# Performance work log

Measured on AMD Instinct MI355X. Metric: run time of the kernel, lower is better.

## Reference

```python
import jax, jax.numpy as jnp
import numpy as np

N_NODES = 100_000
N_EDGES = 1_600_000
F_IN = 64
H = 200
N_GRAPHS = 512
BN_EPS = 1e-5


def setup_inputs() -> dict:
    key = jax.random.key(0)
    ks = jax.random.split(key, 16)

    def w(k, shape):
        fan_in = shape[0]
        return jax.random.normal(k, shape, jnp.float32) / np.sqrt(fan_in)

    return {
        "x": jax.random.normal(ks[0], (N_NODES, F_IN), jnp.float32),
        "edge_index": jax.random.randint(ks[1], (2, N_EDGES), 0, N_NODES),
        "batch": jnp.sort(jax.random.randint(ks[2], (N_NODES,), 0, N_GRAPHS)),
        "eps1": jnp.zeros((), jnp.float32),
        "W1a": w(ks[3], (F_IN, H)), "b1a": jnp.zeros((H,), jnp.float32),
        "W1b": w(ks[4], (H, H)),    "b1b": jnp.zeros((H,), jnp.float32),
        "bn1_gamma": jnp.ones((H,), jnp.float32), "bn1_beta": jnp.zeros((H,), jnp.float32),
        "bn1_mean": 0.1 * jax.random.normal(ks[5], (H,), jnp.float32),
        "bn1_var": jax.random.uniform(ks[6], (H,), jnp.float32, 0.5, 1.5),
        "eps2": jnp.zeros((), jnp.float32),
        "W2a": w(ks[7], (H, H)), "b2a": jnp.zeros((H,), jnp.float32),
        "W2b": w(ks[8], (H, H)), "b2b": jnp.zeros((H,), jnp.float32),
        "bn2_gamma": jnp.ones((H,), jnp.float32), "bn2_beta": jnp.zeros((H,), jnp.float32),
        "bn2_mean": 0.1 * jax.random.normal(ks[9], (H,), jnp.float32),
        "bn2_var": jax.random.uniform(ks[10], (H,), jnp.float32, 0.5, 1.5),
        "Wfc": w(ks[11], (2 * H, 2)), "bfc": jnp.zeros((2,), jnp.float32),
    }


def _gin_conv(x, edge_index, eps, Wa, ba, Wb, bb):
    # GINConv: MLP((1+eps)*x + sum_{j in N(i)} x_j); messages flow src->dst
    src, dst = edge_index[0], edge_index[1]
    agg = jax.ops.segment_sum(x[src], dst, num_segments=x.shape[0])  # [N, d]
    h = (1.0 + eps) * x + agg
    return jax.nn.relu(h @ Wa + ba) @ Wb + bb


def _bn_eval(h, gamma, beta, mean, var):
    return (h - mean) * jax.lax.rsqrt(var + BN_EPS) * gamma + beta


def reference(x, edge_index, batch, eps1, W1a, b1a, W1b, b1b,
              bn1_gamma, bn1_beta, bn1_mean, bn1_var,
              eps2, W2a, b2a, W2b, b2b,
              bn2_gamma, bn2_beta, bn2_mean, bn2_var, Wfc, bfc):
    # dropout in eval mode == identity
    h = jax.nn.relu(_gin_conv(x, edge_index, eps1, W1a, b1a, W1b, b1b))
    h = _bn_eval(h, bn1_gamma, bn1_beta, bn1_mean, bn1_var)
    h = jax.nn.relu(_gin_conv(h, edge_index, eps2, W2a, b2a, W2b, b2b))
    h = _bn_eval(h, bn2_gamma, bn2_beta, bn2_mean, bn2_var)
    pooled_sum = jax.ops.segment_sum(h, batch, num_segments=N_GRAPHS)   # [G, H]
    pooled_max = jax.ops.segment_max(h, batch, num_segments=N_GRAPHS)  # [G, H]
    pooled = jnp.concatenate([pooled_sum, pooled_max], axis=1)          # [G, 2H]
    return jax.nn.log_softmax(pooled @ Wfc + bfc, axis=1)               # [G, 2]
```

## Files before the change

### kernel.cpp

```cpp
#include <hip/hip_runtime.h>
#include <hip/hip_bf16.h>
#include <math.h>

#define N_NODES 100000
#define N_EDGES 1600000
#define F_IN 64
#define H_DIM 200
#define N_GRAPHS 512
#define NB_SCAN 98

#define WT_PER (224 * 224)
#define SA 232

typedef __attribute__((ext_vector_type(8))) short short8v;
typedef __attribute__((ext_vector_type(4))) float f32x4;

__global__ void hist_kernel(const int* __restrict__ ei, int* __restrict__ cnt) {
    int i = blockIdx.x * blockDim.x + threadIdx.x;
    if (i < N_EDGES) atomicAdd(&cnt[ei[N_EDGES + i]], 1);
}

__global__ __launch_bounds__(256) void scan_part(const int* __restrict__ deg,
                                                 int* __restrict__ bsums) {
    int b = blockIdx.x, t = threadIdx.x;
    int i0 = b * 1024 + t * 4;
    int s = 0;
    #pragma unroll
    for (int k = 0; k < 4; ++k) { int i = i0 + k; if (i < N_NODES) s += deg[i]; }
    #pragma unroll
    for (int off = 32; off > 0; off >>= 1) s += __shfl_down(s, off, 64);
    __shared__ int wsum[4];
    if ((t & 63) == 0) wsum[t >> 6] = s;
    __syncthreads();
    if (t == 0) bsums[b] = wsum[0] + wsum[1] + wsum[2] + wsum[3];
}

__global__ void scan_tops(int* __restrict__ bsums, int* __restrict__ ptr) {
    __shared__ int sh[128];
    int t = threadIdx.x;
    int v = (t < NB_SCAN) ? bsums[t] : 0;
    sh[t] = v;
    __syncthreads();
    for (int off = 1; off < 128; off <<= 1) {
        int a = sh[t];
        int add = (t >= off) ? sh[t - off] : 0;
        __syncthreads();
        sh[t] = a + add;
        __syncthreads();
    }
    if (t < NB_SCAN) bsums[t] = sh[t] - v;
    if (t == 127) ptr[N_NODES] = sh[127];
}

__global__ __launch_bounds__(256) void scan_fin(int* __restrict__ deg_cursor,
                                                const int* __restrict__ bsums,
                                                int* __restrict__ ptr) {
    int b = blockIdx.x, t = threadIdx.x;
    int i0 = b * 1024 + t * 4;
    int d[4]; int s = 0;
    #pragma unroll
    for (int k = 0; k < 4; ++k) {
        int i = i0 + k;
        d[k] = (i < N_NODES) ? deg_cursor[i] : 0;
        s += d[k];
    }
    __shared__ int sh[256];
    sh[t] = s;
    __syncthreads();
    for (int off = 1; off < 256; off <<= 1) {
        int a = sh[t];
        int add = (t >= off) ? sh[t - off] : 0;
        __syncthreads();
        sh[t] = a + add;
        __syncthreads();
    }
    int run = bsums[b] + sh[t] - s;
    #pragma unroll
    for (int k = 0; k < 4; ++k) {
        int i = i0 + k;
        if (i < N_NODES) { ptr[i] = run; deg_cursor[i] = run; run += d[k]; }
    }
}

__global__ void fill_kernel(const int* __restrict__ ei, int* __restrict__ cursor,
                            int* __restrict__ csr_src) {
    int i = blockIdx.x * blockDim.x + threadIdx.x;
    if (i < N_EDGES) {
        int s = ei[i];
        int d = ei[N_EDGES + i];
        int p = atomicAdd(&cursor[d], 1);
        csr_src[p] = s;
    }
}

__device__ __forceinline__ short f2bf(float f) {
    __hip_bfloat16 h = __float2bfloat16(f);
    return *reinterpret_cast<const short*>(&h);
}
__device__ __forceinline__ float bf2f(short s) {
    return __uint_as_float(((unsigned)(unsigned short)s) << 16);
}
__device__ __forceinline__ float4 bf4_to_f4(uint2 u) {
    float4 r;
    r.x = __uint_as_float(u.x << 16);
    r.y = __uint_as_float(u.x & 0xffff0000u);
    r.z = __uint_as_float(u.y << 16);
    r.w = __uint_as_float(u.y & 0xffff0000u);
    return r;
}

__global__ void prep_x(const float* __restrict__ X, short* __restrict__ Xb) {
    int i = blockIdx.x * 256 + threadIdx.x;
    if (i < N_NODES * 64) Xb[i] = f2bf(X[i]);
}

__global__ void prep_w(const float* __restrict__ W1a, const float* __restrict__ W1b,
                       const float* __restrict__ W2a, const float* __restrict__ W2b,
                       short* __restrict__ wt) {
    int idx = blockIdx.x * 256 + threadIdx.x;
    if (idx >= 4 * WT_PER) return;
    int tsel = idx / WT_PER, rem = idx % WT_PER;
    int c = rem / 224, k = rem % 224;
    const float* W = (tsel == 0) ? W1a : (tsel == 1) ? W1b : (tsel == 2) ? W2a : W2b;
    int K = (tsel == 0) ? 64 : 200;
    float v = (k < K && c < 200) ? W[k * 200 + c] : 0.0f;
    short hi = f2bf(v);
    short lo = f2bf(v - bf2f(hi));
    wt[(2 * tsel) * WT_PER + rem] = hi;
    wt[(2 * tsel + 1) * WT_PER + rem] = lo;
}

template <int NKS>
__device__ __forceinline__ void gemm_split(const short* __restrict__ SLh,
                                           const short* __restrict__ SLl,
                                           const short* __restrict__ Wh,
                                           const short* __restrict__ Wl,
                                           int l15, int lhi, int rt,
                                           int base, int cnt, f32x4 acc[4]) {
    for (int ks = 0; ks < NKS; ++ks) {
        const int k0 = ks * 32 + 8 * lhi;
        short8v ah = *reinterpret_cast<const short8v*>(SLh + (rt * 16 + l15) * SA + k0);
        short8v al = *reinterpret_cast<const short8v*>(SLl + (rt * 16 + l15) * SA + k0);
        #pragma unroll
        for (int i = 0; i < 4; ++i) {
            if (i < cnt) {
                const int wrow = (base + i) * 16 + l15;
                short8v bh = *reinterpret_cast<const short8v*>(Wh + wrow * 224 + k0);
                short8v bl = *reinterpret_cast<const short8v*>(Wl + wrow * 224 + k0);
                acc[i] = __builtin_amdgcn_mfma_f32_16x16x32_bf16(ah, bh, acc[i], 0, 0, 0);
                acc[i] = __builtin_amdgcn_mfma_f32_16x16x32_bf16(ah, bl, acc[i], 0, 0, 0);
                acc[i] = __builtin_amdgcn_mfma_f32_16x16x32_bf16(al, bh, acc[i], 0, 0, 0);
            }
        }
    }
}

template <bool FIRST>
__global__ __launch_bounds__(1024, 8) void gin_mfma(
        const void* __restrict__ Xv,
        const int* __restrict__ ptr, const int* __restrict__ srcl,
        const float* __restrict__ eps_p,
        const short* __restrict__ Wa2,
        const float* __restrict__ ba,
        const short* __restrict__ Wb2, const float* __restrict__ bb,
        const float* __restrict__ gamma, const float* __restrict__ beta,
        const float* __restrict__ mean, const float* __restrict__ var,
        void* __restrict__ outv) {
    __shared__ __align__(16) short SLh[64 * SA];
    __shared__ __align__(16) short SLl[64 * SA];
    const int t = threadIdx.x;
    const int lane = t & 63;
    const int wid = t >> 6;
    const int node0 = blockIdx.x * 64;
    const float ep = 1.0f + eps_p[0];

    for (int i = t; i < 64 * 32; i += 1024) {
        int row = i >> 5, c = 200 + (i & 31);
        SLh[row * SA + c] = 0;
        SLl[row * SA + c] = 0;
    }

    if (FIRST) {
        const short* Xb = (const short*)Xv;
        for (int rr = 0; rr < 4; ++rr) {
            int row = wid * 4 + rr;
            int node = node0 + row;
            if (node >= N_NODES) break;
            int b = ptr[node], e = ptr[node + 1];
            float a0 = ep * bf2f(Xb[(size_t)node * 64 + lane]);
            float a1 = 0.f;
            int j = b;
            for (; j + 4 <= e; j += 4) {
                int s0 = srcl[j+0], s1 = srcl[j+1], s2 = srcl[j+2], s3 = srcl[j+3];
                short f0 = Xb[(size_t)s0 * 64 + lane];
                short f1 = Xb[(size_t)s1 * 64 + lane];
                short f2 = Xb[(size_t)s2 * 64 + lane];
                short f3 = Xb[(size_t)s3 * 64 + lane];
                a0 += bf2f(f0) + bf2f(f2);
                a1 += bf2f(f1) + bf2f(f3);
            }
            for (; j < e; ++j) a0 += bf2f(Xb[(size_t)srcl[j] * 64 + lane]);
            float s = a0 + a1;
            short hi = f2bf(s);
            SLh[row * SA + lane] = hi;
            SLl[row * SA + lane] = f2bf(s - bf2f(hi));
        }
    } else {
        const uint2* H2 = (const uint2*)Xv;
        for (int rr = 0; rr < 4; ++rr) {
            int row = wid * 4 + rr;
            int node = node0 + row;
            if (node >= N_NODES) break;
            int b = ptr[node], e = ptr[node + 1];
            if (lane < 50) {
                float4 fs = bf4_to_f4(H2[(size_t)node * 50 + lane]);
                float4 A0 = make_float4(ep * fs.x, ep * fs.y, ep * fs.z, ep * fs.w);
                float4 A1 = make_float4(0.f, 0.f, 0.f, 0.f);
                int j = b;
                for (; j + 4 <= e; j += 4) {
                    int s0 = srcl[j+0], s1 = srcl[j+1], s2 = srcl[j+2], s3 = srcl[j+3];
                    uint2 u0 = H2[(size_t)s0 * 50 + lane];
                    uint2 u1 = H2[(size_t)s1 * 50 + lane];
                    uint2 u2 = H2[(size_t)s2 * 50 + lane];
                    uint2 u3 = H2[(size_t)s3 * 50 + lane];
                    float4 f0 = bf4_to_f4(u0), f1 = bf4_to_f4(u1);
                    float4 f2 = bf4_to_f4(u2), f3 = bf4_to_f4(u3);
                    A0.x += f0.x + f2.x; A0.y += f0.y + f2.y;
                    A0.z += f0.z + f2.z; A0.w += f0.w + f2.w;
                    A1.x += f1.x + f3.x; A1.y += f1.y + f3.y;
                    A1.z += f1.z + f3.z; A1.w += f1.w + f3.w;
                }
                for (; j < e; ++j) {
                    float4 f0 = bf4_to_f4(H2[(size_t)srcl[j] * 50 + lane]);
                    A0.x += f0.x; A0.y += f0.y; A0.z += f0.z; A0.w += f0.w;
                }
                float sx = A0.x + A1.x;
                float sy = A0.y + A1.y;
                float sz = A0.z + A1.z;
                float sw = A0.w + A1.w;
                short4 ph, pl;
                ph.x = f2bf(sx); pl.x = f2bf(sx - bf2f(ph.x));
                ph.y = f2bf(sy); pl.y = f2bf(sy - bf2f(ph.y));
                ph.z = f2bf(sz); pl.z = f2bf(sz - bf2f(ph.z));
                ph.w = f2bf(sw); pl.w = f2bf(sw - bf2f(ph.w));
                *reinterpret_cast<short4*>(&SLh[row * SA + 4 * lane]) = ph;
                *reinterpret_cast<short4*>(&SLl[row * SA + 4 * lane]) = pl;
            }
        }
    }
    __syncthreads();

    const int l15 = lane & 15;
    const int lhi = lane >> 4;
    const int rt = wid >> 2;
    const int cq = wid & 3;
    const int base = (cq == 0) ? 0 : (4 + 3 * (cq - 1));
    const int cnt  = (cq == 0) ? 4 : 3;

    f32x4 acc[4];

    #pragma unroll
    for (int i = 0; i < 4; ++i) acc[i] = (f32x4){0.f, 0.f, 0.f, 0.f};
    if (FIRST) gemm_split<2>(SLh, SLl, Wa2, Wa2 + WT_PER, l15, lhi, rt, base, cnt, acc);
    else       gemm_split<7>(SLh, SLl, Wa2, Wa2 + WT_PER, l15, lhi, rt, base, cnt, acc);
    __syncthreads();

    #pragma unroll
    for (int i = 0; i < 4; ++i) {
        if (i < cnt) {
            int col = (base + i) * 16 + l15;
            if (col < 200) {
                float bv = ba[col];
                #pragma unroll
                for (int r = 0; r < 4; ++r) {
                    int row = rt * 16 + lhi * 4 + r;
                    float v = fmaxf(acc[i][r] + bv, 0.0f);
                    short hi = f2bf(v);
                    SLh[row * SA + col] = hi;
                    SLl[row * SA + col] = f2bf(v - bf2f(hi));
                }
            }
        }
    }
    __syncthreads();

    #pragma unroll
    for (int i = 0; i < 4; ++i) acc[i] = (f32x4){0.f, 0.f, 0.f, 0.f};
    gemm_split<7>(SLh, SLl, Wb2, Wb2 + WT_PER, l15, lhi, rt, base, cnt, acc);

    #pragma unroll
    for (int i = 0; i < 4; ++i) {
        if (i < cnt) {
            int col = (base + i) * 16 + l15;
            if (col < 200) {
                float bv = bb[col];
                float g0 = gamma[col], bt = beta[col], mn = mean[col];
                float inv = rsqrtf(var[col] + 1e-5f);
                #pragma unroll
                for (int r = 0; r < 4; ++r) {
                    int row = rt * 16 + lhi * 4 + r;
                    int node = node0 + row;
                    if (node < N_NODES) {
                        float v = fmaxf(acc[i][r] + bv, 0.0f);
                        v = (v - mn) * inv * g0 + bt;
                        if (FIRST) ((__hip_bfloat16*)outv)[(size_t)node * 200 + col] = __float2bfloat16(v);
                        else       ((float*)outv)[(size_t)node * 200 + col] = v;
                    }
                }
            }
        }
    }
}

__device__ __forceinline__ int lower_bound_dev(const int* a, int n, int v) {
    int lo = 0, hi = n;
    while (lo < hi) { int mid = (lo + hi) >> 1; if (a[mid] < v) lo = mid + 1; else hi = mid; }
    return lo;
}

__global__ __launch_bounds__(256) void pool_fc_kernel(const float* __restrict__ h,
        const int* __restrict__ batch, const float* __restrict__ Wfc,
        const float* __restrict__ bfc, float* __restrict__ out) {
    int g = blockIdx.x;
    __shared__ int range[2];
    if (threadIdx.x == 0) range[0] = lower_bound_dev(batch, N_NODES, g);
    else if (threadIdx.x == 64) range[1] = lower_bound_dev(batch, N_NODES, g + 1);
    __syncthreads();
    int b = range[0], e = range[1];
    int d = threadIdx.x;
    float s0 = 0.f, s1 = 0.f, s2 = 0.f, s3 = 0.f, m = -3.0e38f;
    int n = b;
    if (d < 200) {
        for (; n + 4 <= e; n += 4) {
            float v0 = h[(size_t)(n+0) * 200 + d];
            float v1 = h[(size_t)(n+1) * 200 + d];
            float v2 = h[(size_t)(n+2) * 200 + d];
            float v3 = h[(size_t)(n+3) * 200 + d];
            s0 += v0; s1 += v1; s2 += v2; s3 += v3;
            m = fmaxf(m, fmaxf(fmaxf(v0, v1), fmaxf(v2, v3)));
        }
        for (; n < e; ++n) {
            float v = h[(size_t)n * 200 + d];
            s0 += v;
            m = fmaxf(m, v);
        }
    }
    float s = (s0 + s1) + (s2 + s3);
    float c0 = 0.f, c1 = 0.f;
    if (d < 200) {
        c0 = s * Wfc[d * 2 + 0] + m * Wfc[(200 + d) * 2 + 0];
        c1 = s * Wfc[d * 2 + 1] + m * Wfc[(200 + d) * 2 + 1];
    }
    #pragma unroll
    for (int off = 32; off > 0; off >>= 1) {
        c0 += __shfl_down(c0, off, 64);
        c1 += __shfl_down(c1, off, 64);
    }
    __shared__ float r0[4], r1[4];
    int wid = threadIdx.x >> 6;
    if ((threadIdx.x & 63) == 0) { r0[wid] = c0; r1[wid] = c1; }
    __syncthreads();
    if (threadIdx.x == 0) {
        float l0 = r0[0] + r0[1] + r0[2] + r0[3] + bfc[0];
        float l1 = r1[0] + r1[1] + r1[2] + r1[3] + bfc[1];
        float mx = fmaxf(l0, l1);
        float lse = mx + logf(expf(l0 - mx) + expf(l1 - mx));
        out[g * 2 + 0] = l0 - lse;
        out[g * 2 + 1] = l1 - lse;
    }
}

extern "C" void kernel_launch(void* const* d_in, const int* in_sizes, int n_in,
                              void* d_out, int out_size, void* d_ws, size_t ws_size,
                              hipStream_t stream) {
    const float* x    = (const float*)d_in[0];
    const int*   ei   = (const int*)d_in[1];
    const int*   batch= (const int*)d_in[2];
    const float* eps1 = (const float*)d_in[3];
    const float* W1a  = (const float*)d_in[4];
    const float* b1a  = (const float*)d_in[5];
    const float* W1b  = (const float*)d_in[6];
    const float* b1b  = (const float*)d_in[7];
    const float* bn1g = (const float*)d_in[8];
    const float* bn1b = (const float*)d_in[9];
    const float* bn1m = (const float*)d_in[10];
    const float* bn1v = (const float*)d_in[11];
    const float* eps2 = (const float*)d_in[12];
    const float* W2a  = (const float*)d_in[13];
    const float* b2a  = (const float*)d_in[14];
    const float* W2b  = (const float*)d_in[15];
    const float* b2b  = (const float*)d_in[16];
    const float* bn2g = (const float*)d_in[17];
    const float* bn2b = (const float*)d_in[18];
    const float* bn2m = (const float*)d_in[19];
    const float* bn2v = (const float*)d_in[20];
    const float* Wfc  = (const float*)d_in[21];
    const float* bfc  = (const float*)d_in[22];
    float* out = (float*)d_out;

    char* ws = (char*)d_ws;
    int* csr_ptr = (int*)(ws + 0);
    int* cursor  = (int*)(ws + 400128);
    int* csr_src = (int*)(ws + 800256);
    short* wt    = (short*)(ws + 7200256);
    short* W1a2 = wt;
    short* W1b2 = wt + 2 * WT_PER;
    short* W2a2 = wt + 4 * WT_PER;
    short* W2b2 = wt + 6 * WT_PER;
    short* Xb    = (short*)(ws + 8003072);
    __hip_bfloat16* h1b = (__hip_bfloat16*)(ws + 20803072);
    float* h2    = (float*)(ws + 60803072);
    int* bsums   = (int*)(ws + 20803072);

    hipMemsetAsync(cursor, 0, N_NODES * sizeof(int), stream);
    hist_kernel<<<(N_EDGES + 255) / 256, 256, 0, stream>>>(ei, cursor);
    scan_part<<<NB_SCAN, 256, 0, stream>>>(cursor, bsums);
    scan_tops<<<1, 128, 0, stream>>>(bsums, csr_ptr);
    scan_fin<<<NB_SCAN, 256, 0, stream>>>(cursor, bsums, csr_ptr);
    fill_kernel<<<(N_EDGES + 255) / 256, 256, 0, stream>>>(ei, cursor, csr_src);
    prep_w<<<(4 * WT_PER + 255) / 256, 256, 0, stream>>>(W1a, W1b, W2a, W2b, wt);
    prep_x<<<(N_NODES * 64 + 255) / 256, 256, 0, stream>>>(x, Xb);

    const int NBLK = (N_NODES + 63) / 64;
    gin_mfma<true><<<NBLK, 1024, 0, stream>>>(Xb, csr_ptr, csr_src, eps1,
            W1a2, b1a, W1b2, b1b, bn1g, bn1b, bn1m, bn1v, h1b);
    gin_mfma<false><<<NBLK, 1024, 0, stream>>>(h1b, csr_ptr, csr_src, eps2,
            W2a2, b2a, W2b2, b2b, bn2g, bn2b, bn2m, bn2v, h2);

    pool_fc_kernel<<<N_GRAPHS, 256, 0, stream>>>(h2, batch, Wfc, bfc, out);
}
```

Measured before the change: 856.5 us.

## Halve GIN block size, widen per-wave column tiles, trim K padding in LDS

The fused GIN kernel moves from 1024 to 512 threads per block. Each wave now computes 7 column tiles for one 16-row slab, so every A fragment loaded from LDS is reused across more MFMAs. The K dimension is cut from 224 to 208 padded columns using a tail step that overlaps k=176..207, and the weights are re-laid out with stride 256 so the tail can read zeroed duplicate entries. This shrinks LDS use and the number of padded MFMAs. The aggregation loop is unrolled to 8 neighbours per iteration to put more gathers in flight, at the cost of more registers (7 accumulators) and lower occupancy.

Result: slower. 1.074 ms (+25.4%).

```diff
diff --git a/kernel.cpp b/kernel.cpp
--- a/kernel.cpp
+++ b/kernel.cpp
@@ -9,8 +9,9 @@
 #define N_GRAPHS 512
 #define NB_SCAN 98
 
-#define WT_PER (224 * 224)
-#define SA 232
+#define WTK 256
+#define WT_PER (224 * WTK)
+#define SA 208
 
 typedef __attribute__((ext_vector_type(8))) short short8v;
 typedef __attribute__((ext_vector_type(4))) float f32x4;
@@ -120,43 +121,66 @@
     int idx = blockIdx.x * 256 + threadIdx.x;
     if (idx >= 4 * WT_PER) return;
     int tsel = idx / WT_PER, rem = idx % WT_PER;
-    int c = rem / 224, k = rem % 224;
+    int c = rem / WTK, kp = rem % WTK;
     const float* W = (tsel == 0) ? W1a : (tsel == 1) ? W1b : (tsel == 2) ? W2a : W2b;
     int K = (tsel == 0) ? 64 : 200;
-    float v = (k < K && c < 200) ? W[k * 200 + c] : 0.0f;
+    int k; bool valid;
+    if (kp < 224) { k = kp; valid = (k < K) && (k < 200); }
+    else { int m = kp - 224; k = 192 + (m - 16); valid = (m >= 16) && (k < K) && (k < 200); }
+    float v = (valid && c < 200) ? W[k * 200 + c] : 0.0f;
     short hi = f2bf(v);
     short lo = f2bf(v - bf2f(hi));
     wt[(2 * tsel) * WT_PER + rem] = hi;
     wt[(2 * tsel + 1) * WT_PER + rem] = lo;
 }
 
-template <int NKS>
+template <int NKS, bool TAIL>
 __device__ __forceinline__ void gemm_split(const short* __restrict__ SLh,
                                            const short* __restrict__ SLl,
                                            const short* __restrict__ Wh,
                                            const short* __restrict__ Wl,
-                                           int l15, int lhi, int rt,
-                                           int base, int cnt, f32x4 acc[4]) {
+                                           int l15, int lhi, int rt, int ch,
+                                           f32x4 acc[7]) {
+    const int arow = (rt * 16 + l15) * SA;
     for (int ks = 0; ks < NKS; ++ks) {
         const int k0 = ks * 32 + 8 * lhi;
-        short8v ah = *reinterpret_cast<const short8v*>(SLh + (rt * 16 + l15) * SA + k0);
-        short8v al = *reinterpret_cast<const short8v*>(SLl + (rt * 16 + l15) * SA + k0);
+        short8v ah = *reinterpret_cast<const short8v*>(SLh + arow + k0);
+        short8v al = *reinterpret_cast<const short8v*>(SLl + arow + k0);
         #pragma unroll
-        for (int i = 0; i < 4; ++i) {
-            if (i < cnt) {
-                const int wrow = (base + i) * 16 + l15;
-                short8v bh = *reinterpret_cast<const short8v*>(Wh + wrow * 224 + k0);
-                short8v bl = *reinterpret_cast<const short8v*>(Wl + wrow * 224 + k0);
-                acc[i] = __builtin_amdgcn_mfma_f32_16x16x32_bf16(ah, bh, acc[i], 0, 0, 0);
-                acc[i] = __builtin_amdgcn_mfma_f32_16x16x32_bf16(ah, bl, acc[i], 0, 0, 0);
-                acc[i] = __builtin_amdgcn_mfma_f32_16x16x32_bf16(al, bh, acc[i], 0, 0, 0);
+        for (int ct = 0; ct < 7; ++ct) {
+            const int tile = ch * 7 + ct;
+            if (tile < 13) {
+                const int wof = (tile * 16 + l15) * WTK + k0;
+                short8v bh = *reinterpret_cast<const short8v*>(Wh + wof);
+                short8v bl = *reinterpret_cast<const short8v*>(Wl + wof);
+                acc[ct] = __builtin_amdgcn_mfma_f32_16x16x32_bf16(ah, bh, acc[ct], 0, 0, 0);
+                acc[ct] = __builtin_amdgcn_mfma_f32_16x16x32_bf16(ah, bl, acc[ct], 0, 0, 0);
+                acc[ct] = __builtin_amdgcn_mfma_f32_16x16x32_bf16(al, bh, acc[ct], 0, 0, 0);
+            }
+        }
+    }
+    if (TAIL) {
+        const int k0a = 176 + 8 * lhi;
+        short8v ah = *reinterpret_cast<const short8v*>(SLh + arow + k0a);
+        short8v al = *reinterpret_cast<const short8v*>(SLl + arow + k0a);
+        const int k0b = 224 + 8 * lhi;
+        #pragma unroll
+        for (int ct = 0; ct < 7; ++ct) {
+            const int tile = ch * 7 + ct;
+            if (tile < 13) {
+                const int wof = (tile * 16 + l15) * WTK + k0b;
+                short8v bh = *reinterpret_cast<const short8v*>(Wh + wof);
+                short8v bl = *reinterpret_cast<const short8v*>(Wl + wof);
+                acc[ct] = __builtin_amdgcn_mfma_f32_16x16x32_bf16(ah, bh, acc[ct], 0, 0, 0);
+                acc[ct] = __builtin_amdgcn_mfma_f32_16x16x32_bf16(ah, bl, acc[ct], 0, 0, 0);
+                acc[ct] = __builtin_amdgcn_mfma_f32_16x16x32_bf16(al, bh, acc[ct], 0, 0, 0);
             }
         }
     }
 }
 
 template <bool FIRST>
-__global__ __launch_bounds__(1024, 8) void gin_mfma(
+__global__ __launch_bounds__(512, 6) void gin_mfma(
         const void* __restrict__ Xv,
         const int* __restrict__ ptr, const int* __restrict__ srcl,
         const float* __restrict__ eps_p,
@@ -174,30 +198,41 @@
     const int node0 = blockIdx.x * 64;
     const float ep = 1.0f + eps_p[0];
 
-    for (int i = t; i < 64 * 32; i += 1024) {
-        int row = i >> 5, c = 200 + (i & 31);
+    {
+        int row = t >> 3, c = 200 + (t & 7);
         SLh[row * SA + c] = 0;
         SLl[row * SA + c] = 0;
     }
 
     if (FIRST) {
         const short* Xb = (const short*)Xv;
-        for (int rr = 0; rr < 4; ++rr) {
-            int row = wid * 4 + rr;
+        for (int rr = 0; rr < 8; ++rr) {
+            int row = wid * 8 + rr;
             int node = node0 + row;
             if (node >= N_NODES) break;
             int b = ptr[node], e = ptr[node + 1];
             float a0 = ep * bf2f(Xb[(size_t)node * 64 + lane]);
             float a1 = 0.f;
             int j = b;
-            for (; j + 4 <= e; j += 4) {
+            for (; j + 8 <= e; j += 8) {
                 int s0 = srcl[j+0], s1 = srcl[j+1], s2 = srcl[j+2], s3 = srcl[j+3];
+                int s4 = srcl[j+4], s5 = srcl[j+5], s6 = srcl[j+6], s7 = srcl[j+7];
                 short f0 = Xb[(size_t)s0 * 64 + lane];
                 short f1 = Xb[(size_t)s1 * 64 + lane];
                 short f2 = Xb[(size_t)s2 * 64 + lane];
                 short f3 = Xb[(size_t)s3 * 64 + lane];
-                a0 += bf2f(f0) + bf2f(f2);
-                a1 += bf2f(f1) + bf2f(f3);
+                short f4 = Xb[(size_t)s4 * 64 + lane];
+                short f5 = Xb[(size_t)s5 * 64 + lane];
+                short f6 = Xb[(size_t)s6 * 64 + lane];
+                short f7 = Xb[(size_t)s7 * 64 + lane];
+                a0 += (bf2f(f0) + bf2f(f2)) + (bf2f(f4) + bf2f(f6));
+                a1 += (bf2f(f1) + bf2f(f3)) + (bf2f(f5) + bf2f(f7));
+            }
+            if (j + 4 <= e) {
+                int s0 = srcl[j+0], s1 = srcl[j+1], s2 = srcl[j+2], s3 = srcl[j+3];
+                a0 += bf2f(Xb[(size_t)s0 * 64 + lane]) + bf2f(Xb[(size_t)s2 * 64 + lane]);
+                a1 += bf2f(Xb[(size_t)s1 * 64 + lane]) + bf2f(Xb[(size_t)s3 * 64 + lane]);
+                j += 4;
             }
             for (; j < e; ++j) a0 += bf2f(Xb[(size_t)srcl[j] * 64 + lane]);
             float s = a0 + a1;
@@ -207,8 +242,8 @@
         }
     } else {
         const uint2* H2 = (const uint2*)Xv;
-        for (int rr = 0; rr < 4; ++rr) {
-            int row = wid * 4 + rr;
+        for (int rr = 0; rr < 8; ++rr) {
+            int row = wid * 8 + rr;
             int node = node0 + row;
             if (node >= N_NODES) break;
             int b = ptr[node], e = ptr[node + 1];
@@ -217,18 +252,41 @@
                 float4 A0 = make_float4(ep * fs.x, ep * fs.y, ep * fs.z, ep * fs.w);
                 float4 A1 = make_float4(0.f, 0.f, 0.f, 0.f);
                 int j = b;
-                for (; j + 4 <= e; j += 4) {
+                for (; j + 8 <= e; j += 8) {
                     int s0 = srcl[j+0], s1 = srcl[j+1], s2 = srcl[j+2], s3 = srcl[j+3];
+                    int s4 = srcl[j+4], s5 = srcl[j+5], s6 = srcl[j+6], s7 = srcl[j+7];
                     uint2 u0 = H2[(size_t)s0 * 50 + lane];
                     uint2 u1 = H2[(size_t)s1 * 50 + lane];
                     uint2 u2 = H2[(size_t)s2 * 50 + lane];
                     uint2 u3 = H2[(size_t)s3 * 50 + lane];
+                    uint2 u4 = H2[(size_t)s4 * 50 + lane];
+                    uint2 u5 = H2[(size_t)s5 * 50 + lane];
+                    uint2 u6 = H2[(size_t)s6 * 50 + lane];
+                    uint2 u7 = H2[(size_t)s7 * 50 + lane];
                     float4 f0 = bf4_to_f4(u0), f1 = bf4_to_f4(u1);
                     float4 f2 = bf4_to_f4(u2), f3 = bf4_to_f4(u3);
+                    float4 f4 = bf4_to_f4(u4), f5 = bf4_to_f4(u5);
+                    float4 f6 = bf4_to_f4(u6), f7 = bf4_to_f4(u7);
+                    A0.x += (f0.x + f2.x) + (f4.x + f6.x);
+                    A0.y += (f0.y + f2.y) + (f4.y + f6.y);
+                    A0.z += (f0.z + f2.z) + (f4.z + f6.z);
+                    A0.w += (f0.w + f2.w) + (f4.w + f6.w);
+                    A1.x += (f1.x + f3.x) + (f5.x + f7.x);
+                    A1.y += (f1.y + f3.y) + (f5.y + f7.y);
+                    A1.z += (f1.z + f3.z) + (f5.z + f7.z);
+                    A1.w += (f1.w + f3.w) + (f5.w + f7.w);
+                }
+                if (j + 4 <= e) {
+                    int s0 = srcl[j+0], s1 = srcl[j+1], s2 = srcl[j+2], s3 = srcl[j+3];
+                    float4 f0 = bf4_to_f4(H2[(size_t)s0 * 50 + lane]);
+                    float4 f1 = bf4_to_f4(H2[(size_t)s1 * 50 + lane]);
+                    float4 f2 = bf4_to_f4(H2[(size_t)s2 * 50 + lane]);
+                    float4 f3 = bf4_to_f4(H2[(size_t)s3 * 50 + lane]);
                     A0.x += f0.x + f2.x; A0.y += f0.y + f2.y;
                     A0.z += f0.z + f2.z; A0.w += f0.w + f2.w;
                     A1.x += f1.x + f3.x; A1.y += f1.y + f3.y;
                     A1.z += f1.z + f3.z; A1.w += f1.w + f3.w;
+                    j += 4;
                 }
                 for (; j < e; ++j) {
                     float4 f0 = bf4_to_f4(H2[(size_t)srcl[j] * 50 + lane]);
@@ -252,61 +310,54 @@
 
     const int l15 = lane & 15;
     const int lhi = lane >> 4;
-    const int rt = wid >> 2;
-    const int cq = wid & 3;
-    const int base = (cq == 0) ? 0 : (4 + 3 * (cq - 1));
-    const int cnt  = (cq == 0) ? 4 : 3;
-
-    f32x4 acc[4];
-
-    #pragma unroll
-    for (int i = 0; i < 4; ++i) acc[i] = (f32x4){0.f, 0.f, 0.f, 0.f};
-    if (FIRST) gemm_split<2>(SLh, SLl, Wa2, Wa2 + WT_PER, l15, lhi, rt, base, cnt, acc);
-    else       gemm_split<7>(SLh, SLl, Wa2, Wa2 + WT_PER, l15, lhi, rt, base, cnt, acc);
-    __syncthreads();
-
-    #pragma unroll
-    for (int i = 0; i < 4; ++i) {
-        if (i < cnt) {
-            int col = (base + i) * 16 + l15;
-            if (col < 200) {
-                float bv = ba[col];
-                #pragma unroll
-                for (int r = 0; r < 4; ++r) {
-                    int row = rt * 16 + lhi * 4 + r;
-                    float v = fmaxf(acc[i][r] + bv, 0.0f);
-                    short hi = f2bf(v);
-                    SLh[row * SA + col] = hi;
-                    SLl[row * SA + col] = f2bf(v - bf2f(hi));
-                }
-            }
-        }
-    }
-    __syncthreads();
-
-    #pragma unroll
-    for (int i = 0; i < 4; ++i) acc[i] = (f32x4){0.f, 0.f, 0.f, 0.f};
-    gemm_split<7>(SLh, SLl, Wb2, Wb2 + WT_PER, l15, lhi, rt, base, cnt, acc);
-
-    #pragma unroll
-    for (int i = 0; i < 4; ++i) {
-        if (i < cnt) {
-            int col = (base + i) * 16 + l15;
-            if (col < 200) {
-                float bv = bb[col];
-                float g0 = gamma[col], bt = beta[col], mn = mean[col];
-                float inv = rsqrtf(var[col] + 1e-5f);
-                #pragma unroll
-                for (int r = 0; r < 4; ++r) {
-                    int row = rt * 16 + lhi * 4 + r;
-                    int node = node0 + row;
-                    if (node < N_NODES) {
-                        float v = fmaxf(acc[i][r] + bv, 0.0f);
-                        v = (v - mn) * inv * g0 + bt;
-                        if (FIRST) ((__hip_bfloat16*)outv)[(size_t)node * 200 + col] = __float2bfloat16(v);
-                        else       ((float*)outv)[(size_t)node * 200 + col] = v;
-                    }
-                }
+    const int rt = wid >> 1;
+    const int ch = wid & 1;
+
+    f32x4 acc[7];
+
+    #pragma unroll
+    for (int i = 0; i < 7; ++i) acc[i] = (f32x4){0.f, 0.f, 0.f, 0.f};
+    if (FIRST) gemm_split<2, false>(SLh, SLl, Wa2, Wa2 + WT_PER, l15, lhi, rt, ch, acc);
+    else       gemm_split<6, true >(SLh, SLl, Wa2, Wa2 + WT_PER, l15, lhi, rt, ch, acc);
+    __syncthreads();
+
+    #pragma unroll
+    for (int i = 0; i < 7; ++i) {
+        int col = (ch * 7 + i) * 16 + l15;
+        if (col < 200) {
+            float bv = ba[col];
+            #pragma unroll
+            for (int r = 0; r < 4; ++r) {
+                int row = rt * 16 + lhi * 4 + r;
+                float v = fmaxf(acc[i][r] + bv, 0.0f);
+                short hi = f2bf(v);
+                SLh[row * SA + col] = hi;
+                SLl[row * SA + col] = f2bf(v - bf2f(hi));
+            }
+        }
+    }
+    __syncthreads();
+
+    #pragma unroll
+    for (int i = 0; i < 7; ++i) acc[i] = (f32x4){0.f, 0.f, 0.f, 0.f};
+    gemm_split<6, true>(SLh, SLl, Wb2, Wb2 + WT_PER, l15, lhi, rt, ch, acc);
+
+    #pragma unroll
+    for (int i = 0; i < 7; ++i) {
+        int col = (ch * 7 + i) * 16 + l15;
+        if (col >= 200) continue;
+        float bv = bb[col];
+        float g0 = gamma[col], bt = beta[col], mn = mean[col];
+        float inv = rsqrtf(var[col] + 1e-5f);
+        #pragma unroll
+        for (int r = 0; r < 4; ++r) {
+            int row = rt * 16 + lhi * 4 + r;
+            int node = node0 + row;
+            if (node < N_NODES) {
+                float v = fmaxf(acc[i][r] + bv, 0.0f);
+                v = (v - mn) * inv * g0 + bt;
+                if (FIRST) ((__hip_bfloat16*)outv)[(size_t)node * 200 + col] = __float2bfloat16(v);
+                else       ((float*)outv)[(size_t)node * 200 + col] = v;
             }
         }
     }
@@ -407,10 +458,10 @@
     short* W1b2 = wt + 2 * WT_PER;
     short* W2a2 = wt + 4 * WT_PER;
     short* W2b2 = wt + 6 * WT_PER;
-    short* Xb    = (short*)(ws + 8003072);
-    __hip_bfloat16* h1b = (__hip_bfloat16*)(ws + 20803072);
-    float* h2    = (float*)(ws + 60803072);
-    int* bsums   = (int*)(ws + 20803072);
+    short* Xb    = (short*)(ws + 8117760);
+    __hip_bfloat16* h1b = (__hip_bfloat16*)(ws + 20917760);
+    float* h2    = (float*)(ws + 60917760);
+    int* bsums   = (int*)(ws + 20917760);
 
     hipMemsetAsync(cursor, 0, N_NODES * sizeof(int), stream);
     hist_kernel<<<(N_EDGES + 255) / 256, 256, 0, stream>>>(ei, cursor);
@@ -422,9 +473,9 @@
     prep_x<<<(N_NODES * 64 + 255) / 256, 256, 0, stream>>>(x, Xb);
 
     const int NBLK = (N_NODES + 63) / 64;
-    gin_mfma<true><<<NBLK, 1024, 0, stream>>>(Xb, csr_ptr, csr_src, eps1,
+    gin_mfma<true><<<NBLK, 512, 0, stream>>>(Xb, csr_ptr, csr_src, eps1,
             W1a2, b1a, W1b2, b1b, bn1g, bn1b, bn1m, bn1v, h1b);
-    gin_mfma<false><<<NBLK, 1024, 0, stream>>>(h1b, csr_ptr, csr_src, eps2,
+    gin_mfma<false><<<NBLK, 512, 0, stream>>>(h1b, csr_ptr, csr_src, eps2,
             W2a2, b2a, W2b2, b2b, bn2g, bn2b, bn2m, bn2v, h2);
 
     pool_fc_kernel<<<N_GRAPHS, 256, 0, stream>>>(h2, batch, Wfc, bfc, out);
```
